# Performance work log

Hardware: AMD Instinct MI355X
Metric: run time of the kernel (lower is better)

## Reference

```python
import jax, jax.numpy as jnp
import numpy as np

N = 50000          # nodes
E = 1_600_000      # edges (avg degree 32)
H = 2              # attention heads per layer
F = 64             # per-head feature dim
NC = 16            # num_classes
NEG_SLOPE = 0.2    # PyG GATConv default leaky relu slope


def setup_inputs():
    key = jax.random.key(0)
    ks = jax.random.split(key, 20)
    s = 0.05
    z = jnp.zeros
    inp = {
        'x': jax.random.normal(ks[0], (N, 64), dtype=jnp.float32),
        'edge_index': jax.random.randint(ks[1], (2, E), 0, N, dtype=jnp.int32),
        # GAT layer 1: in=64 (heads=1 concat from input), out=H*F
        'W1': jax.random.normal(ks[2], (64, H * F)) * s,
        'a_src1': jax.random.normal(ks[3], (H, F)) * s,
        'a_dst1': jax.random.normal(ks[4], (H, F)) * s,
        'b1': z((H * F,)),
        # GAT layer 2: in=H*F=128, out=H*F
        'W2': jax.random.normal(ks[5], (H * F, H * F)) * s,
        'a_src2': jax.random.normal(ks[6], (H, F)) * s,
        'a_dst2': jax.random.normal(ks[7], (H, F)) * s,
        'b2': z((H * F,)),
        # MLP head: 128 -> 512 -> 256 -> NC
        'lw1': jax.random.normal(ks[8], (H * F, 512)) * s, 'lb1': z((512,)),
        'lw2': jax.random.normal(ks[9], (512, 256)) * s, 'lb2': z((256,)),
        'lw3': jax.random.normal(ks[10], (256, NC)) * s, 'lb3': z((NC,)),
    }
    return inp


def gat_conv(x, src, dst, W, a_src, a_dst, b):
    """PyG-style GATConv (shared weights for src/dst), head concat output."""
    h = (x @ W).reshape(-1, H, F)                       # [N, H, F]
    alpha_s = jnp.einsum('nhf,hf->nh', h, a_src)        # [N, H]
    alpha_d = jnp.einsum('nhf,hf->nh', h, a_dst)
    e = jax.nn.leaky_relu(alpha_s[src] + alpha_d[dst], NEG_SLOPE)  # [E', H]
    # segment softmax over incoming edges of each dst node
    e_max = jax.ops.segment_max(e, dst, num_segments=N)            # [N, H]
    e_exp = jnp.exp(e - e_max[dst])
    denom = jax.ops.segment_sum(e_exp, dst, num_segments=N)
    alpha = e_exp / (denom[dst] + 1e-16)                            # [E', H]
    msg = h[src] * alpha[:, :, None]                                # [E', H, F]
    out = jax.ops.segment_sum(msg, dst, num_segments=N)             # [N, H, F]
    return out.reshape(N, H * F) + b


def reference(x, edge_index, W1, a_src1, a_dst1, b1, W2, a_src2, a_dst2, b2,
              lw1, lb1, lw2, lb2, lw3, lb3):
    # add self loops (PyG GATConv default)
    loop = jnp.arange(N, dtype=edge_index.dtype)
    src = jnp.concatenate([edge_index[0], loop])
    dst = jnp.concatenate([edge_index[1], loop])

    h = jax.nn.relu(gat_conv(x, src, dst, W1, a_src1, a_dst1, b1))
    emb = jax.nn.relu(gat_conv(h, src, dst, W2, a_src2, a_dst2, b2))

    z = jax.nn.relu(emb @ lw1 + lb1)
    z = jax.nn.relu(z @ lw2 + lb2)
    logits = z @ lw3 + lb3
    return emb, logits
```

## Files before the change

kernel.cpp:

```cpp
#include <hip/hip_runtime.h>

typedef __bf16 bf16f __attribute__((ext_vector_type(8)));
typedef float  f32x4 __attribute__((ext_vector_type(4)));

__device__ __forceinline__ float bf2f(unsigned short u) {
  union { unsigned int u; float f; } v;
  v.u = ((unsigned int)u) << 16;
  return v.f;
}
__device__ __forceinline__ unsigned short f2bf(float f) {
  union { float f; unsigned int u; } v; v.f = f;
  unsigned int r = v.u + 0x7FFFu + ((v.u >> 16) & 1u);
  return (unsigned short)(r >> 16);
}
__device__ __forceinline__ float bflo(unsigned int w) {
  union { unsigned int u; float f; } v; v.u = w << 16; return v.f;
}
__device__ __forceinline__ float bfhi(unsigned int w) {
  union { unsigned int u; float f; } v; v.u = w & 0xFFFF0000u; return v.f;
}

__global__ void GNNModel_general_12077448036407_kernel(int* cnt, int ncnt) {
  int i = blockIdx.x * blockDim.x + threadIdx.x;
  if (i < ncnt) cnt[i] = 0;
}

__global__ void wpack2_kernel(const float* __restrict__ lw1, unsigned short* __restrict__ Wb1,
                              const float* __restrict__ lw2, unsigned short* __restrict__ Wb2) {
  int i = blockIdx.x * blockDim.x + threadIdx.x;
  if (i < 512 * 128) {
    int n = i >> 7, k = i & 127;
    Wb1[i] = f2bf(lw1[(size_t)k * 512 + n]);
  }
  if (i < 256 * 512) {
    int n = i >> 9, k = i & 511;
    Wb2[i] = f2bf(lw2[(size_t)k * 256 + n]);
  }
}

__launch_bounds__(256)
__global__ void gr_fused_kernel(const float* __restrict__ x, const float* __restrict__ W1,
                                unsigned short* __restrict__ hb, int M, int gblocks,
                                const int* __restrict__ dst, int* __restrict__ cnt,
                                unsigned short* __restrict__ rank, int E) {
  __shared__ float As[16][132];
  __shared__ float Bs[16][136];
  int bid = blockIdx.x;
  int t = threadIdx.x;

  if (bid >= gblocks) {
    int e = (bid - gblocks) * 256 + t;
    if (e < E) {
      int r = atomicAdd(&cnt[dst[e]], 1);
      rank[e] = (unsigned short)r;
    }
    return;
  }

  int tx = t & 15, ty = t >> 4;
  int m0 = bid * 128;

  float acc[8][8];
#pragma unroll
  for (int i = 0; i < 8; i++)
#pragma unroll
    for (int j = 0; j < 8; j++) acc[i][j] = 0.0f;

  int arow = t >> 1;
  int akc  = (t & 1) * 8;
  int bkk  = t >> 4;
  int bnn  = (t & 15) * 8;
  int gm = m0 + arow;

  for (int k0 = 0; k0 < 64; k0 += 16) {
    float av[8];
    if (gm < M) {
      const float* Af = x + (size_t)gm * 64 + k0 + akc;
      float4 r0 = *(const float4*)Af;
      float4 r1 = *(const float4*)(Af + 4);
      av[0] = r0.x; av[1] = r0.y; av[2] = r0.z; av[3] = r0.w;
      av[4] = r1.x; av[5] = r1.y; av[6] = r1.z; av[7] = r1.w;
    } else {
#pragma unroll
      for (int j = 0; j < 8; j++) av[j] = 0.0f;
    }
#pragma unroll
    for (int j = 0; j < 8; j++) As[akc + j][arow] = av[j];

    const float* bp = W1 + (size_t)(k0 + bkk) * 128 + bnn;
    float4 b0 = *(const float4*)bp;
    float4 b1 = *(const float4*)(bp + 4);
    *(float4*)&Bs[bkk][bnn]     = b0;
    *(float4*)&Bs[bkk][bnn + 4] = b1;

    __syncthreads();

#pragma unroll 4
    for (int kk = 0; kk < 16; kk++) {
      float a[8], b[8];
      *(float4*)&a[0] = *(const float4*)&As[kk][ty * 8];
      *(float4*)&a[4] = *(const float4*)&As[kk][ty * 8 + 4];
      *(float4*)&b[0] = *(const float4*)&Bs[kk][tx * 8];
      *(float4*)&b[4] = *(const float4*)&Bs[kk][tx * 8 + 4];
#pragma unroll
      for (int i = 0; i < 8; i++)
#pragma unroll
        for (int j = 0; j < 8; j++)
          acc[i][j] = fmaf(a[i], b[j], acc[i][j]);
    }
    __syncthreads();
  }

#pragma unroll
  for (int i = 0; i < 8; i++) {
    int m = m0 + ty * 8 + i;
    if (m >= M) continue;
    unsigned short* Cp = hb + (size_t)m * 128 + tx * 8;
    uint4 pk;
    pk.x = (unsigned int)f2bf(acc[i][0]) | ((unsigned int)f2bf(acc[i][1]) << 16);
    pk.y = (unsigned int)f2bf(acc[i][2]) | ((unsigned int)f2bf(acc[i][3]) << 16);
    pk.z = (unsigned int)f2bf(acc[i][4]) | ((unsigned int)f2bf(acc[i][5]) << 16);
    pk.w = (unsigned int)f2bf(acc[i][6]) | ((unsigned int)f2bf(acc[i][7]) << 16);
    *(uint4*)Cp = pk;
  }
}

__global__ void scan1_kernel(const int* __restrict__ cnt, int* __restrict__ offs,
                             int* __restrict__ bsum, int M) {
  __shared__ int sh[256];
  int t = threadIdx.x;
  int i = blockIdx.x * 256 + t;
  int v = (i < M) ? cnt[i] : 0;
  sh[t] = v;
  __syncthreads();
  for (int off = 1; off < 256; off <<= 1) {
    int u = (t >= off) ? sh[t - off] : 0;
    __syncthreads();
    sh[t] += u;
    __syncthreads();
  }
  if (i <= M) offs[i] = sh[t] - v;
  if (t == 255) bsum[blockIdx.x] = sh[255];
}

__global__ void scan2_kernel(int* __restrict__ bsum, int NB) {
  __shared__ int sh[256];
  int t = threadIdx.x;
  int v = (t < NB) ? bsum[t] : 0;
  sh[t] = v;
  __syncthreads();
  for (int off = 1; off < 256; off <<= 1) {
    int u = (t >= off) ? sh[t - off] : 0;
    __syncthreads();
    sh[t] += u;
    __syncthreads();
  }
  if (t < NB) bsum[t] = sh[t] - v;
}

__global__ void scan3_kernel(int* __restrict__ offs, const int* __restrict__ bsum, int M) {
  int i = blockIdx.x * 256 + threadIdx.x;
  if (i <= M) offs[i] += bsum[i >> 8];
}

__global__ void pa_fused_kernel(const unsigned short* __restrict__ hb,
                                const float* __restrict__ a_src,
                                const float* __restrict__ a_dst,
                                float2* __restrict__ aSp, float2* __restrict__ aDp,
                                int M, int ablocks,
                                const int* __restrict__ src, const int* __restrict__ dstp,
                                const unsigned short* __restrict__ rank,
                                const int* __restrict__ offs, int* __restrict__ csr, int E) {
  int bid = blockIdx.x;
  int t = threadIdx.x;

  if (bid >= ablocks) {
    int e = (bid - ablocks) * 256 + t;
    if (e < E) {
      int p = offs[dstp[e]] + (int)rank[e];
      __builtin_nontemporal_store(src[e], &csr[p]);
    }
    return;
  }

  int gw = (bid * 256 + t) >> 6;
  int lane = t & 63;
  if (gw >= M) return;
  float h0 = bf2f(hb[(size_t)gw * 128 + lane]);
  float h1 = bf2f(hb[(size_t)gw * 128 + 64 + lane]);
  float as0 = h0 * a_src[lane];
  float as1 = h1 * a_src[64 + lane];
  float ad0 = h0 * a_dst[lane];
  float ad1 = h1 * a_dst[64 + lane];
  for (int o = 32; o; o >>= 1) {
    as0 += __shfl_xor(as0, o);
    as1 += __shfl_xor(as1, o);
    ad0 += __shfl_xor(ad0, o);
    ad1 += __shfl_xor(ad1, o);
  }
  if (lane == 0) {
    aSp[gw] = make_float2(as0, as1);
    aDp[gw] = make_float2(ad0, ad1);
  }
}

__launch_bounds__(256)
__global__ void m128_kernel(const void* __restrict__ A,
                            const unsigned short* __restrict__ Bw,
                            const float* __restrict__ bias, void* __restrict__ C,
                            int M, int K, int Nt, int aBF, int cBF, int relu,
                            int mtiles, int lgNB) {
  __shared__ unsigned short sh[8704];
  unsigned short* As = sh;
  unsigned short* Bs = sh + 4096;
  int tid = threadIdx.x;
  int wid = tid >> 6, lane = tid & 63;
  int lm = lane & 15, quad = lane >> 4;
  int wr = wid >> 1, wc = wid & 1;

  int xcd = blockIdx.x;
  int slot = blockIdx.y;
  int qm = mtiles >> 3, rm = mtiles & 7;
  int cntm = qm + (xcd < rm);
  int mstart = xcd * qm + (xcd < rm ? xcd : rm);
  if (slot >= (cntm << lgNB)) return;
  int NBm1 = (1 << lgNB) - 1;
  int m0 = (mstart + (slot >> lgNB)) * 128;
  int n0 = (slot & NBm1) * 128;

  f32x4 acc[4][4];
#pragma unroll
  for (int mi = 0; mi < 4; mi++)
#pragma unroll
    for (int ni = 0; ni < 4; ni++)
#pragma unroll
      for (int i = 0; i < 4; i++) acc[mi][ni][i] = 0.0f;

  int c0 = (wid << 6) + lane;
  int c1 = c0 + 256;
  int srow = tid >> 1;
  int skc  = (tid & 1) << 4;

  for (int k0 = 0; k0 < K; k0 += 32) {
    {
      const unsigned short* g0 = Bw + (size_t)(n0 + (c0 >> 2)) * K + k0 + ((c0 & 3) << 3);
      __builtin_amdgcn_global_load_lds((const __attribute__((address_space(1))) void*)g0,
                                       (__attribute__((address_space(3))) void*)(Bs + (wid << 9)),
                                       16, 0, 0);
      const unsigned short* g1 = Bw + (size_t)(n0 + (c1 >> 2)) * K + k0 + ((c1 & 3) << 3);
      __builtin_amdgcn_global_load_lds((const __attribute__((address_space(1))) void*)g1,
                                       (__attribute__((address_space(3))) void*)(Bs + 2048 + (wid << 9)),
                                       16, 0, 0);
    }
    if (aBF) {
      int r0 = m0 + (c0 >> 2); if (r0 > M - 1) r0 = M - 1;
      const unsigned short* g0 = (const unsigned short*)A + (size_t)r0 * K + k0 + ((c0 & 3) << 3);
      __builtin_amdgcn_global_load_lds((const __attribute__((address_space(1))) void*)g0,
                                       (__attribute__((address_space(3))) void*)(As + (wid << 9)),
                                       16, 0, 0);
      int r1 = m0 + (c1 >> 2); if (r1 > M - 1) r1 = M - 1;
      const unsigned short* g1 = (const unsigned short*)A + (size_t)r1 * K + k0 + ((c1 & 3) << 3);
      __builtin_amdgcn_global_load_lds((const __attribute__((address_space(1))) void*)g1,
                                       (__attribute__((address_space(3))) void*)(As + 2048 + (wid << 9)),
                                       16, 0, 0);
    } else {
      int gm = m0 + srow;
      uint4 p0, p1;
      if (gm < M) {
        const float* Af = (const float*)A + (size_t)gm * K + k0 + skc;
        float4 r0 = *(const float4*)Af;
        float4 r1 = *(const float4*)(Af + 4);
        float4 r2 = *(const float4*)(Af + 8);
        float4 r3 = *(const float4*)(Af + 12);
        p0.x = (unsigned int)f2bf(r0.x) | ((unsigned int)f2bf(r0.y) << 16);
        p0.y = (unsigned int)f2bf(r0.z) | ((unsigned int)f2bf(r0.w) << 16);
        p0.z = (unsigned int)f2bf(r1.x) | ((unsigned int)f2bf(r1.y) << 16);
        p0.w = (unsigned int)f2bf(r1.z) | ((unsigned int)f2bf(r1.w) << 16);
        p1.x = (unsigned int)f2bf(r2.x) | ((unsigned int)f2bf(r2.y) << 16);
        p1.y = (unsigned int)f2bf(r2.z) | ((unsigned int)f2bf(r2.w) << 16);
        p1.z = (unsigned int)f2bf(r3.x) | ((unsigned int)f2bf(r3.y) << 16);
        p1.w = (unsigned int)f2bf(r3.z) | ((unsigned int)f2bf(r3.w) << 16);
      } else {
        p0.x = p0.y = p0.z = p0.w = 0u;
        p1.x = p1.y = p1.z = p1.w = 0u;
      }
      *(uint4*)&As[srow * 32 + skc] = p0;
      *(uint4*)&As[srow * 32 + skc + 8] = p1;
    }
    __syncthreads();

    bf16f afr[4], bfr[4];
#pragma unroll
    for (int mi = 0; mi < 4; mi++)
      afr[mi] = *(const bf16f*)&As[(wr * 64 + mi * 16 + lm) * 32 + quad * 8];
#pragma unroll
    for (int ni = 0; ni < 4; ni++)
      bfr[ni] = *(const bf16f*)&Bs[(wc * 64 + ni * 16 + lm) * 32 + quad * 8];
#pragma unroll
    for (int mi = 0; mi < 4; mi++)
#pragma unroll
      for (int ni = 0; ni < 4; ni++)
        acc[mi][ni] = __builtin_amdgcn_mfma_f32_16x16x32_bf16(afr[mi], bfr[ni], acc[mi][ni], 0, 0, 0);
    __syncthreads();
  }

  if (cBF) {
#pragma unroll
    for (int p = 0; p < 2; p++) {
      __syncthreads();
      if (wc == p) {
#pragma unroll
        for (int ni = 0; ni < 4; ni++) {
          int colb = ni * 16 + lm;
          float bv = (bias != 0) ? bias[n0 + p * 64 + colb] : 0.0f;
#pragma unroll
          for (int mi = 0; mi < 4; mi++) {
#pragma unroll
            for (int i = 0; i < 4; i++) {
              int rowb = wr * 64 + mi * 16 + quad * 4 + i;
              float v = acc[mi][ni][i] + bv;
              if (relu) v = fmaxf(v, 0.0f);
              sh[rowb * 68 + colb] = f2bf(v);
            }
          }
        }
      }
      __syncthreads();
#pragma unroll
      for (int sweep = 0; sweep < 4; sweep++) {
        int rowb = (tid >> 3) + 32 * sweep;
        int seg = tid & 7;
        int grow = m0 + rowb;
        if (grow < M) {
          uint4 val = *(const uint4*)&sh[rowb * 68 + seg * 8];
          *(uint4*)((unsigned short*)C + (size_t)grow * Nt + n0 + p * 64 + seg * 8) = val;
        }
      }
    }
  } else {
#pragma unroll
    for (int ni = 0; ni < 4; ni++) {
      int col = n0 + wc * 64 + ni * 16 + lm;
      float bv = (bias != 0) ? bias[col] : 0.0f;
#pragma unroll
      for (int mi = 0; mi < 4; mi++) {
#pragma unroll
        for (int i = 0; i < 4; i++) {
          int row = m0 + wr * 64 + mi * 16 + quad * 4 + i;
          if (row < M) {
            float v = acc[mi][ni][i] + bv;
            if (relu) v = fmaxf(v, 0.0f);
            ((float*)C)[(size_t)row * Nt + col] = v;
          }
        }
      }
    }
  }
}

__launch_bounds__(256)
__global__ void lgemm_kernel(const unsigned short* __restrict__ A,
                             const float* __restrict__ W,
                             const float* __restrict__ bias, float* __restrict__ C,
                             int M, int K) {
  __shared__ unsigned short Bt[16 * 264];
  int tid = threadIdx.x;
  int wave = tid >> 6, lane = tid & 63;
  int lm = lane & 15, quad = lane >> 4;
  int m0 = blockIdx.x * 64;

  for (int f0 = tid * 4; f0 < K * 16; f0 += 1024) {
    float4 w4 = *(const float4*)(W + f0);
    int k = f0 >> 4, n = f0 & 15;
    Bt[(n + 0) * 264 + k] = f2bf(w4.x);
    Bt[(n + 1) * 264 + k] = f2bf(w4.y);
    Bt[(n + 2) * 264 + k] = f2bf(w4.z);
    Bt[(n + 3) * 264 + k] = f2bf(w4.w);
  }
  __syncthreads();

  f32x4 acc;
#pragma unroll
  for (int i = 0; i < 4; i++) acc[i] = 0.0f;

  int m = m0 + wave * 16 + lm;
  const unsigned short* Ap = A + (size_t)m * K;

  for (int k0 = 0; k0 < K; k0 += 32) {
    bf16f af;
#pragma unroll
    for (int j = 0; j < 8; j++) af[j] = (__bf16)0.0f;
    if (m < M) af = *(const bf16f*)(Ap + k0 + quad * 8);
    bf16f bfv = *(const bf16f*)&Bt[lm * 264 + k0 + quad * 8];
    acc = __builtin_amdgcn_mfma_f32_16x16x32_bf16(af, bfv, acc, 0, 0, 0);
  }

  float bv = bias[lm];
#pragma unroll
  for (int i = 0; i < 4; i++) {
    int row = m0 + wave * 16 + quad * 4 + i;
    if (row < M) C[(size_t)row * 16 + lm] = acc[i] + bv;
  }
}

__launch_bounds__(256)
__global__ void tgemm_kernel(const void* __restrict__ A, const float* __restrict__ W,
                             const float* __restrict__ bias, void* __restrict__ C,
                             int M, int K, int Nt, int aBF, int cBF, int relu) {
  __shared__ float As[16][132];
  __shared__ float Bs[16][136];
  int t = threadIdx.x;
  int tx = t & 15, ty = t >> 4;
  int m0 = blockIdx.x * 128, n0 = blockIdx.y * 128;

  float acc[8][8];
#pragma unroll
  for (int i = 0; i < 8; i++)
#pragma unroll
    for (int j = 0; j < 8; j++) acc[i][j] = 0.0f;

  int arow = t >> 1;
  int akc  = (t & 1) * 8;
  int bkk  = t >> 4;
  int bnn  = (t & 15) * 8;
  int gm = m0 + arow;

  for (int k0 = 0; k0 < K; k0 += 16) {
    float av[8];
    if (gm < M) {
      if (aBF) {
        const unsigned short* Ab = (const unsigned short*)A + (size_t)gm * K + k0 + akc;
        uint4 raw = *(const uint4*)Ab;
        av[0] = bflo(raw.x); av[1] = bfhi(raw.x);
        av[2] = bflo(raw.y); av[3] = bfhi(raw.y);
        av[4] = bflo(raw.z); av[5] = bfhi(raw.z);
        av[6] = bflo(raw.w); av[7] = bfhi(raw.w);
      } else {
        const float* Af = (const float*)A + (size_t)gm * K + k0 + akc;
        float4 r0 = *(const float4*)Af;
        float4 r1 = *(const float4*)(Af + 4);
        av[0] = r0.x; av[1] = r0.y; av[2] = r0.z; av[3] = r0.w;
        av[4] = r1.x; av[5] = r1.y; av[6] = r1.z; av[7] = r1.w;
      }
    } else {
#pragma unroll
      for (int j = 0; j < 8; j++) av[j] = 0.0f;
    }
#pragma unroll
    for (int j = 0; j < 8; j++) As[akc + j][arow] = av[j];

    const float* bp = W + (size_t)(k0 + bkk) * Nt + n0 + bnn;
    float4 b0 = *(const float4*)bp;
    float4 b1 = *(const float4*)(bp + 4);
    *(float4*)&Bs[bkk][bnn]     = b0;
    *(float4*)&Bs[bkk][bnn + 4] = b1;

    __syncthreads();

#pragma unroll 4
    for (int kk = 0; kk < 16; kk++) {
      float a[8], b[8];
      *(float4*)&a[0] = *(const float4*)&As[kk][ty * 8];
      *(float4*)&a[4] = *(const float4*)&As[kk][ty * 8 + 4];
      *(float4*)&b[0] = *(const float4*)&Bs[kk][tx * 8];
      *(float4*)&b[4] = *(const float4*)&Bs[kk][tx * 8 + 4];
#pragma unroll
      for (int i = 0; i < 8; i++)
#pragma unroll
        for (int j = 0; j < 8; j++)
          acc[i][j] = fmaf(a[i], b[j], acc[i][j]);
    }
    __syncthreads();
  }

  float bv[8];
#pragma unroll
  for (int j = 0; j < 8; j++) bv[j] = (bias != 0) ? bias[n0 + tx * 8 + j] : 0.0f;

#pragma unroll
  for (int i = 0; i < 8; i++) {
    int m = m0 + ty * 8 + i;
    if (m >= M) continue;
    float v[8];
#pragma unroll
    for (int j = 0; j < 8; j++) {
      float s = acc[i][j] + bv[j];
      v[j] = relu ? fmaxf(s, 0.0f) : s;
    }
    if (cBF) {
      unsigned short* Cp = (unsigned short*)C + (size_t)m * Nt + n0 + tx * 8;
      uint4 pk;
      pk.x = (unsigned int)f2bf(v[0]) | ((unsigned int)f2bf(v[1]) << 16);
      pk.y = (unsigned int)f2bf(v[2]) | ((unsigned int)f2bf(v[3]) << 16);
      pk.z = (unsigned int)f2bf(v[4]) | ((unsigned int)f2bf(v[5]) << 16);
      pk.w = (unsigned int)f2bf(v[6]) | ((unsigned int)f2bf(v[7]) << 16);
      *(uint4*)Cp = pk;
    } else {
      float* Cp = (float*)C + (size_t)m * Nt + n0 + tx * 8;
      float4 o0; o0.x = v[0]; o0.y = v[1]; o0.z = v[2]; o0.w = v[3];
      float4 o1; o1.x = v[4]; o1.y = v[5]; o1.z = v[6]; o1.w = v[7];
      *(float4*)Cp = o0;
      *(float4*)(Cp + 4) = o1;
    }
  }
}

__global__ void alphas_kernel(const unsigned short* __restrict__ hb,
                              const float* __restrict__ a_src,
                              const float* __restrict__ a_dst,
                              float2* __restrict__ aSp, float2* __restrict__ aDp, int M) {
  int gw = (blockIdx.x * blockDim.x + threadIdx.x) >> 6;
  int lane = threadIdx.x & 63;
  if (gw >= M) return;
  float h0 = bf2f(hb[(size_t)gw * 128 + lane]);
  float h1 = bf2f(hb[(size_t)gw * 128 + 64 + lane]);
  float as0 = h0 * a_src[lane];
  float as1 = h1 * a_src[64 + lane];
  float ad0 = h0 * a_dst[lane];
  float ad1 = h1 * a_dst[64 + lane];
  for (int o = 32; o; o >>= 1) {
    as0 += __shfl_xor(as0, o);
    as1 += __shfl_xor(as1, o);
    ad0 += __shfl_xor(ad0, o);
    ad1 += __shfl_xor(ad1, o);
  }
  if (lane == 0) {
    aSp[gw] = make_float2(as0, as1);
    aDp[gw] = make_float2(ad0, ad1);
  }
}

__global__ void aggregate_kernel(const unsigned short* __restrict__ hb,
                                 const float2* __restrict__ aSp,
                                 const float2* __restrict__ aDp,
                                 const int* __restrict__ csr_src, const int* __restrict__ offs,
                                 const float* __restrict__ bias,
                                 float* __restrict__ out, int M) {
  int n = (blockIdx.x * blockDim.x + threadIdx.x) >> 6;
  int lane = threadIdx.x & 63;
  if (n >= M) return;
  int g = lane >> 4;
  int q = lane & 15;
  int h0sel = (q < 8);

  float2 adn = aDp[n];
  float2 asn = aSp[n];
  float e0 = asn.x + adn.x; e0 = (e0 > 0.0f) ? e0 : 0.2f * e0;
  float e1 = asn.y + adn.y; e1 = (e1 > 0.0f) ? e1 : 0.2f * e1;
  float ws0 = expf(e0), ws1 = expf(e1);
  float wself = h0sel ? ws0 : ws1;

  float acc[8];
  if (g == 0) {
    uint4 rv = *(const uint4*)(hb + (size_t)n * 128 + q * 8);
    acc[0] = wself * bflo(rv.x); acc[1] = wself * bfhi(rv.x);
    acc[2] = wself * bflo(rv.y); acc[3] = wself * bfhi(rv.y);
    acc[4] = wself * bflo(rv.z); acc[5] = wself * bfhi(rv.z);
    acc[6] = wself * bflo(rv.w); acc[7] = wself * bfhi(rv.w);
  } else {
#pragma unroll
    for (int i = 0; i < 8; i++) acc[i] = 0.0f;
  }

  float lp0 = 0.0f, lp1 = 0.0f;
  int rs = offs[n], re = offs[n + 1];
  for (int base = rs; base < re; base += 64) {
    int cnt = re - base; if (cnt > 64) cnt = 64;
    int s = 0; float w0 = 0.0f, w1 = 0.0f;
    if (lane < cnt) {
      s = csr_src[base + lane];
      float2 a = aSp[s];
      float f0 = a.x + adn.x; f0 = (f0 > 0.0f) ? f0 : 0.2f * f0;
      float f1 = a.y + adn.y; f1 = (f1 > 0.0f) ? f1 : 0.2f * f1;
      w0 = expf(f0); w1 = expf(f1);
      lp0 += w0; lp1 += w1;
    }
    int jmax = (cnt + 3) >> 2;
#pragma unroll 2
    for (int j = 0; j < jmax; j++) {
      int el = 4 * j + g;
      int sj  = __shfl(s, el);
      float w0j = __shfl(w0, el);
      float w1j = __shfl(w1, el);
      float wj = h0sel ? w0j : w1j;
      uint4 rv = *(const uint4*)(hb + (size_t)sj * 128 + q * 8);
      acc[0] = fmaf(wj, bflo(rv.x), acc[0]);
      acc[1] = fmaf(wj, bfhi(rv.x), acc[1]);
      acc[2] = fmaf(wj, bflo(rv.y), acc[2]);
      acc[3] = fmaf(wj, bfhi(rv.y), acc[3]);
      acc[4] = fmaf(wj, bflo(rv.z), acc[4]);
      acc[5] = fmaf(wj, bfhi(rv.z), acc[5]);
      acc[6] = fmaf(wj, bflo(rv.w), acc[6]);
      acc[7] = fmaf(wj, bfhi(rv.w), acc[7]);
    }
  }
#pragma unroll
  for (int i = 0; i < 8; i++) {
    acc[i] += __shfl_xor(acc[i], 16);
    acc[i] += __shfl_xor(acc[i], 32);
  }
  for (int o = 32; o; o >>= 1) {
    lp0 += __shfl_xor(lp0, o);
    lp1 += __shfl_xor(lp1, o);
  }
  if (g == 0) {
    float linv = 1.0f / ((h0sel ? lp0 + ws0 : lp1 + ws1) + 1e-16f);
    const float* bp = bias + q * 8;
    float4 o0, o1;
    o0.x = fmaxf(acc[0] * linv + bp[0], 0.0f);
    o0.y = fmaxf(acc[1] * linv + bp[1], 0.0f);
    o0.z = fmaxf(acc[2] * linv + bp[2], 0.0f);
    o0.w = fmaxf(acc[3] * linv + bp[3], 0.0f);
    o1.x = fmaxf(acc[4] * linv + bp[4], 0.0f);
    o1.y = fmaxf(acc[5] * linv + bp[5], 0.0f);
    o1.z = fmaxf(acc[6] * linv + bp[6], 0.0f);
    o1.w = fmaxf(acc[7] * linv + bp[7], 0.0f);
    float* op = out + (size_t)n * 128 + q * 8;
    *(float4*)op = o0;
    *(float4*)(op + 4) = o1;
  }
}

extern "C" void kernel_launch(void* const* d_in, const int* in_sizes, int n_in,
                              void* d_out, int out_size, void* d_ws, size_t ws_size,
                              hipStream_t stream) {
  const int N = in_sizes[0] / 64;
  const int E = in_sizes[1] / 2;
  const float* x   = (const float*)d_in[0];
  const int*   ei  = (const int*)d_in[1];
  const float* W1  = (const float*)d_in[2];
  const float* as1 = (const float*)d_in[3];
  const float* ad1 = (const float*)d_in[4];
  const float* b1  = (const float*)d_in[5];
  const float* W2  = (const float*)d_in[6];
  const float* as2 = (const float*)d_in[7];
  const float* ad2 = (const float*)d_in[8];
  const float* b2  = (const float*)d_in[9];
  const float* lw1 = (const float*)d_in[10];
  const float* lb1 = (const float*)d_in[11];
  const float* lw2 = (const float*)d_in[12];
  const float* lb2 = (const float*)d_in[13];
  const float* lw3 = (const float*)d_in[14];
  const float* lb3 = (const float*)d_in[15];

  float* emb    = (float*)d_out;
  float* logits = (float*)d_out + (size_t)N * 128;

  char* base = (char*)d_ws;
  size_t o = 0;
  unsigned short* Wb1 = (unsigned short*)(base + o); o += ((size_t)512 * 128 * 2 + 255) & ~(size_t)255;
  unsigned short* Wb2 = (unsigned short*)(base + o); o += ((size_t)256 * 512 * 2 + 255) & ~(size_t)255;
  char* tb = base + o;

  size_t t = 0;
  unsigned short* hb = (unsigned short*)(tb + t); t += ((size_t)N * 128 * 2 + 255) & ~(size_t)255;
  float* x2f = (float*)(tb + t); t += ((size_t)N * 128 * 4 + 255) & ~(size_t)255;
  float2* aSp = (float2*)(tb + t); t += ((size_t)N * 8 + 255) & ~(size_t)255;
  float2* aDp = (float2*)(tb + t); t += ((size_t)N * 8 + 255) & ~(size_t)255;
  int* cnt  = (int*)(tb + t); t += ((size_t)N * 4 + 255) & ~(size_t)255;
  int* offs = (int*)(tb + t); t += ((size_t)(N + 1) * 4 + 255) & ~(size_t)255;
  int* bsum = (int*)(tb + t); t += ((size_t)256 * 4 + 255) & ~(size_t)255;
  unsigned short* rank = (unsigned short*)(tb + t); t += ((size_t)E * 2 + 255) & ~(size_t)255;
  int* csr  = (int*)(tb + t); t += ((size_t)E * 4 + 255) & ~(size_t)255;
  unsigned short* z1b = (unsigned short*)tb;
  unsigned short* z2b = (unsigned short*)(tb + (((size_t)N * 512 * 2 + 255) & ~(size_t)255));

  const int* esrc = ei;
  const int* edst = ei + E;

  int eb = (E + 255) / 256;
  int sb = (N + 256) / 256;
  int nb4 = (N + 3) / 4;
  int mtb = (N + 127) / 128;

  GNNModel_general_12077448036407_kernel<<<(N + 255) / 256, 256, 0, stream>>>(cnt, N);
  wpack2_kernel<<<512, 256, 0, stream>>>(lw1, Wb1, lw2, Wb2);

  gr_fused_kernel<<<mtb + eb, 256, 0, stream>>>(x, W1, hb, N, mtb, edst, cnt, rank, E);

  scan1_kernel<<<sb, 256, 0, stream>>>(cnt, offs, bsum, N);
  scan2_kernel<<<1, 256, 0, stream>>>(bsum, sb);
  scan3_kernel<<<sb, 256, 0, stream>>>(offs, bsum, N);

  pa_fused_kernel<<<nb4 + eb, 256, 0, stream>>>(hb, as1, ad1, aSp, aDp, N, nb4,
                                                esrc, edst, rank, offs, csr, E);

  aggregate_kernel<<<nb4, 256, 0, stream>>>(hb, aSp, aDp, csr, offs, b1, x2f, N);

  tgemm_kernel<<<dim3(mtb, 1), 256, 0, stream>>>(x2f, W2, (const float*)0, hb,
                                                 N, 128, 128, 0, 1, 0);
  alphas_kernel<<<nb4, 256, 0, stream>>>(hb, as2, ad2, aSp, aDp, N);
  aggregate_kernel<<<nb4, 256, 0, stream>>>(hb, aSp, aDp, csr, offs, b2, emb, N);

  int qx = mtb >> 3, rx = mtb & 7;
  int spx = qx + (rx ? 1 : 0);
  m128_kernel<<<dim3(8, spx * 4), 256, 0, stream>>>(emb, Wb1, lb1, z1b,
                                                    N, 128, 512, 0, 1, 1, mtb, 2);
  m128_kernel<<<dim3(8, spx * 2), 256, 0, stream>>>(z1b, Wb2, lb2, z2b,
                                                    N, 512, 256, 1, 1, 1, mtb, 1);
  int mtb64 = (N + 63) / 64;
  lgemm_kernel<<<mtb64, 256, 0, stream>>>(z2b, lw3, lb3, logits, N, 256);
}
```

Before: 467.6 us.

## Fuse attention logits into GEMM epilogues and use split-bf16 MFMA for layer-2 GEMM

Measured after the change: 442.6 us. 5.3% less time.

```diff
diff --git a/kernel.cpp b/kernel.cpp
--- a/kernel.cpp
+++ b/kernel.cpp
@@ -25,8 +25,10 @@
   if (i < ncnt) cnt[i] = 0;
 }
 
-__global__ void wpack2_kernel(const float* __restrict__ lw1, unsigned short* __restrict__ Wb1,
-                              const float* __restrict__ lw2, unsigned short* __restrict__ Wb2) {
+__global__ void wpack3_kernel(const float* __restrict__ lw1, unsigned short* __restrict__ Wb1,
+                              const float* __restrict__ lw2, unsigned short* __restrict__ Wb2,
+                              const float* __restrict__ W2, unsigned short* __restrict__ W2h,
+                              unsigned short* __restrict__ W2l) {
   int i = blockIdx.x * blockDim.x + threadIdx.x;
   if (i < 512 * 128) {
     int n = i >> 7, k = i & 127;
@@ -36,11 +38,21 @@
     int n = i >> 9, k = i & 511;
     Wb2[i] = f2bf(lw2[(size_t)k * 256 + n]);
   }
+  if (i < 128 * 128) {
+    int n = i >> 7, k = i & 127;
+    float w = W2[(size_t)k * 128 + n];
+    unsigned short h = f2bf(w);
+    W2h[i] = h;
+    W2l[i] = f2bf(w - bf2f(h));
+  }
 }
 
 __launch_bounds__(256)
 __global__ void gr_fused_kernel(const float* __restrict__ x, const float* __restrict__ W1,
-                                unsigned short* __restrict__ hb, int M, int gblocks,
+                                unsigned short* __restrict__ hb,
+                                const float* __restrict__ a_src, const float* __restrict__ a_dst,
+                                float2* __restrict__ aSp, float2* __restrict__ aDp,
+                                int M, int gblocks,
                                 const int* __restrict__ dst, int* __restrict__ cnt,
                                 unsigned short* __restrict__ rank, int E) {
   __shared__ float As[16][132];
@@ -111,17 +123,48 @@
     __syncthreads();
   }
 
+  float aSv[8], aDv[8];
+  {
+    float4 s0 = *(const float4*)(a_src + tx * 8);
+    float4 s1 = *(const float4*)(a_src + tx * 8 + 4);
+    aSv[0]=s0.x; aSv[1]=s0.y; aSv[2]=s0.z; aSv[3]=s0.w;
+    aSv[4]=s1.x; aSv[5]=s1.y; aSv[6]=s1.z; aSv[7]=s1.w;
+    float4 d0 = *(const float4*)(a_dst + tx * 8);
+    float4 d1 = *(const float4*)(a_dst + tx * 8 + 4);
+    aDv[0]=d0.x; aDv[1]=d0.y; aDv[2]=d0.z; aDv[3]=d0.w;
+    aDv[4]=d1.x; aDv[5]=d1.y; aDv[6]=d1.z; aDv[7]=d1.w;
+  }
+
 #pragma unroll
   for (int i = 0; i < 8; i++) {
     int m = m0 + ty * 8 + i;
-    if (m >= M) continue;
-    unsigned short* Cp = hb + (size_t)m * 128 + tx * 8;
-    uint4 pk;
-    pk.x = (unsigned int)f2bf(acc[i][0]) | ((unsigned int)f2bf(acc[i][1]) << 16);
-    pk.y = (unsigned int)f2bf(acc[i][2]) | ((unsigned int)f2bf(acc[i][3]) << 16);
-    pk.z = (unsigned int)f2bf(acc[i][4]) | ((unsigned int)f2bf(acc[i][5]) << 16);
-    pk.w = (unsigned int)f2bf(acc[i][6]) | ((unsigned int)f2bf(acc[i][7]) << 16);
-    *(uint4*)Cp = pk;
+    float asP = 0.0f, adP = 0.0f;
+    if (m < M) {
+      uint4 pk;
+      pk.x = (unsigned int)f2bf(acc[i][0]) | ((unsigned int)f2bf(acc[i][1]) << 16);
+      pk.y = (unsigned int)f2bf(acc[i][2]) | ((unsigned int)f2bf(acc[i][3]) << 16);
+      pk.z = (unsigned int)f2bf(acc[i][4]) | ((unsigned int)f2bf(acc[i][5]) << 16);
+      pk.w = (unsigned int)f2bf(acc[i][6]) | ((unsigned int)f2bf(acc[i][7]) << 16);
+      *(uint4*)(hb + (size_t)m * 128 + tx * 8) = pk;
+      float av[8];
+      av[0] = bflo(pk.x); av[1] = bfhi(pk.x);
+      av[2] = bflo(pk.y); av[3] = bfhi(pk.y);
+      av[4] = bflo(pk.z); av[5] = bfhi(pk.z);
+      av[6] = bflo(pk.w); av[7] = bfhi(pk.w);
+#pragma unroll
+      for (int j = 0; j < 8; j++) {
+        asP = fmaf(av[j], aSv[j], asP);
+        adP = fmaf(av[j], aDv[j], adP);
+      }
+    }
+    asP += __shfl_xor(asP, 1); asP += __shfl_xor(asP, 2); asP += __shfl_xor(asP, 4);
+    adP += __shfl_xor(adP, 1); adP += __shfl_xor(adP, 2); adP += __shfl_xor(adP, 4);
+    float asO = __shfl_xor(asP, 8);
+    float adO = __shfl_xor(adP, 8);
+    if (m < M && tx == 0) {
+      aSp[m] = make_float2(asP, asO);
+      aDp[m] = make_float2(adP, adO);
+    }
   }
 }
 
@@ -163,44 +206,13 @@
   if (i <= M) offs[i] += bsum[i >> 8];
 }
 
-__global__ void pa_fused_kernel(const unsigned short* __restrict__ hb,
-                                const float* __restrict__ a_src,
-                                const float* __restrict__ a_dst,
-                                float2* __restrict__ aSp, float2* __restrict__ aDp,
-                                int M, int ablocks,
-                                const int* __restrict__ src, const int* __restrict__ dstp,
-                                const unsigned short* __restrict__ rank,
-                                const int* __restrict__ offs, int* __restrict__ csr, int E) {
-  int bid = blockIdx.x;
-  int t = threadIdx.x;
-
-  if (bid >= ablocks) {
-    int e = (bid - ablocks) * 256 + t;
-    if (e < E) {
-      int p = offs[dstp[e]] + (int)rank[e];
-      __builtin_nontemporal_store(src[e], &csr[p]);
-    }
-    return;
-  }
-
-  int gw = (bid * 256 + t) >> 6;
-  int lane = t & 63;
-  if (gw >= M) return;
-  float h0 = bf2f(hb[(size_t)gw * 128 + lane]);
-  float h1 = bf2f(hb[(size_t)gw * 128 + 64 + lane]);
-  float as0 = h0 * a_src[lane];
-  float as1 = h1 * a_src[64 + lane];
-  float ad0 = h0 * a_dst[lane];
-  float ad1 = h1 * a_dst[64 + lane];
-  for (int o = 32; o; o >>= 1) {
-    as0 += __shfl_xor(as0, o);
-    as1 += __shfl_xor(as1, o);
-    ad0 += __shfl_xor(ad0, o);
-    ad1 += __shfl_xor(ad1, o);
-  }
-  if (lane == 0) {
-    aSp[gw] = make_float2(as0, as1);
-    aDp[gw] = make_float2(ad0, ad1);
+__global__ void place_kernel(const int* __restrict__ src, const int* __restrict__ dst,
+                             const unsigned short* __restrict__ rank,
+                             const int* __restrict__ offs, int* __restrict__ csr_src, int E) {
+  int e = blockIdx.x * blockDim.x + threadIdx.x;
+  if (e < E) {
+    int p = offs[dst[e]] + (int)rank[e];
+    __builtin_nontemporal_store(src[e], &csr_src[p]);
   }
 }
 
@@ -359,6 +371,172 @@
 }
 
 __launch_bounds__(256)
+__global__ void tg2m_kernel(const float* __restrict__ A,
+                            const unsigned short* __restrict__ Bh,
+                            const unsigned short* __restrict__ Bl,
+                            const float* __restrict__ a_src, const float* __restrict__ a_dst,
+                            unsigned short* __restrict__ hb,
+                            float2* __restrict__ aSp, float2* __restrict__ aDp,
+                            int M) {
+  __shared__ unsigned short sh[12288];
+  unsigned short* Ah = sh;
+  unsigned short* Al = sh + 2048;
+  unsigned short* BH = sh + 4096;
+  unsigned short* BL = sh + 8192;
+  const int K = 128;
+  int tid = threadIdx.x;
+  int wid = tid >> 6, lane = tid & 63;
+  int lm = lane & 15, quad = lane >> 4;
+  int wr = wid >> 1, wc = wid & 1;
+  int m0 = blockIdx.x * 64;
+
+  f32x4 acc[2][4];
+#pragma unroll
+  for (int mi = 0; mi < 2; mi++)
+#pragma unroll
+    for (int ni = 0; ni < 4; ni++)
+#pragma unroll
+      for (int i = 0; i < 4; i++) acc[mi][ni][i] = 0.0f;
+
+  int c0 = (wid << 6) + lane, c1 = c0 + 256;
+  int srow = tid >> 2;
+  int skc = (tid & 3) << 3;
+
+  for (int k0 = 0; k0 < K; k0 += 32) {
+    {
+      const unsigned short* g0 = Bh + (size_t)(c0 >> 2) * K + k0 + ((c0 & 3) << 3);
+      __builtin_amdgcn_global_load_lds((const __attribute__((address_space(1))) void*)g0,
+                                       (__attribute__((address_space(3))) void*)(BH + (wid << 9)),
+                                       16, 0, 0);
+      const unsigned short* g1 = Bh + (size_t)(c1 >> 2) * K + k0 + ((c1 & 3) << 3);
+      __builtin_amdgcn_global_load_lds((const __attribute__((address_space(1))) void*)g1,
+                                       (__attribute__((address_space(3))) void*)(BH + 2048 + (wid << 9)),
+                                       16, 0, 0);
+      const unsigned short* g2 = Bl + (size_t)(c0 >> 2) * K + k0 + ((c0 & 3) << 3);
+      __builtin_amdgcn_global_load_lds((const __attribute__((address_space(1))) void*)g2,
+                                       (__attribute__((address_space(3))) void*)(BL + (wid << 9)),
+                                       16, 0, 0);
+      const unsigned short* g3 = Bl + (size_t)(c1 >> 2) * K + k0 + ((c1 & 3) << 3);
+      __builtin_amdgcn_global_load_lds((const __attribute__((address_space(1))) void*)g3,
+                                       (__attribute__((address_space(3))) void*)(BL + 2048 + (wid << 9)),
+                                       16, 0, 0);
+    }
+    {
+      int gm = m0 + srow;
+      uint4 ph, pl;
+      if (gm < M) {
+        const float* Af = A + (size_t)gm * K + k0 + skc;
+        float4 r0 = *(const float4*)Af;
+        float4 r1 = *(const float4*)(Af + 4);
+        float v[8] = {r0.x, r0.y, r0.z, r0.w, r1.x, r1.y, r1.z, r1.w};
+        unsigned short hh[8], ll[8];
+#pragma unroll
+        for (int j = 0; j < 8; j++) {
+          hh[j] = f2bf(v[j]);
+          ll[j] = f2bf(v[j] - bf2f(hh[j]));
+        }
+        ph.x = (unsigned int)hh[0] | ((unsigned int)hh[1] << 16);
+        ph.y = (unsigned int)hh[2] | ((unsigned int)hh[3] << 16);
+        ph.z = (unsigned int)hh[4] | ((unsigned int)hh[5] << 16);
+        ph.w = (unsigned int)hh[6] | ((unsigned int)hh[7] << 16);
+        pl.x = (unsigned int)ll[0] | ((unsigned int)ll[1] << 16);
+        pl.y = (unsigned int)ll[2] | ((unsigned int)ll[3] << 16);
+        pl.z = (unsigned int)ll[4] | ((unsigned int)ll[5] << 16);
+        pl.w = (unsigned int)ll[6] | ((unsigned int)ll[7] << 16);
+      } else {
+        ph.x = ph.y = ph.z = ph.w = 0u;
+        pl.x = pl.y = pl.z = pl.w = 0u;
+      }
+      *(uint4*)&Ah[srow * 32 + skc] = ph;
+      *(uint4*)&Al[srow * 32 + skc] = pl;
+    }
+    __syncthreads();
+
+    bf16f ahf[2], alf[2];
+#pragma unroll
+    for (int mi = 0; mi < 2; mi++) {
+      ahf[mi] = *(const bf16f*)&Ah[(wr * 32 + mi * 16 + lm) * 32 + quad * 8];
+      alf[mi] = *(const bf16f*)&Al[(wr * 32 + mi * 16 + lm) * 32 + quad * 8];
+    }
+#pragma unroll
+    for (int ni = 0; ni < 4; ni++) {
+      bf16f vbh = *(const bf16f*)&BH[(wc * 64 + ni * 16 + lm) * 32 + quad * 8];
+      bf16f vbl = *(const bf16f*)&BL[(wc * 64 + ni * 16 + lm) * 32 + quad * 8];
+#pragma unroll
+      for (int mi = 0; mi < 2; mi++) {
+        acc[mi][ni] = __builtin_amdgcn_mfma_f32_16x16x32_bf16(ahf[mi], vbh, acc[mi][ni], 0, 0, 0);
+        acc[mi][ni] = __builtin_amdgcn_mfma_f32_16x16x32_bf16(alf[mi], vbh, acc[mi][ni], 0, 0, 0);
+        acc[mi][ni] = __builtin_amdgcn_mfma_f32_16x16x32_bf16(ahf[mi], vbl, acc[mi][ni], 0, 0, 0);
+      }
+    }
+    __syncthreads();
+  }
+
+  float ps[2], pd[2];
+#pragma unroll
+  for (int p = 0; p < 2; p++) {
+    __syncthreads();
+    if (wc == p) {
+#pragma unroll
+      for (int ni = 0; ni < 4; ni++) {
+        int colb = ni * 16 + lm;
+#pragma unroll
+        for (int mi = 0; mi < 2; mi++)
+#pragma unroll
+          for (int i = 0; i < 4; i++) {
+            int rowb = wr * 32 + mi * 16 + quad * 4 + i;
+            sh[rowb * 72 + colb] = f2bf(acc[mi][ni][i]);
+          }
+      }
+    }
+    __syncthreads();
+#pragma unroll
+    for (int sweep = 0; sweep < 2; sweep++) {
+      int rowb = (tid >> 3) + 32 * sweep;
+      int seg = tid & 7;
+      int grow = m0 + rowb;
+      if (grow < M) {
+        uint4 val = *(const uint4*)&sh[rowb * 72 + seg * 8];
+        *(uint4*)(hb + (size_t)grow * 128 + p * 64 + seg * 8) = val;
+      }
+    }
+    {
+      int row = tid >> 2, sg = tid & 3;
+      const float* As_ = a_src + p * 64 + sg * 16;
+      const float* Ad_ = a_dst + p * 64 + sg * 16;
+      float s = 0.0f, d = 0.0f;
+#pragma unroll
+      for (int c8 = 0; c8 < 2; c8++) {
+        uint4 rv = *(const uint4*)&sh[row * 72 + sg * 16 + c8 * 8];
+        const float* Ap_ = As_ + c8 * 8;
+        const float* Dp_ = Ad_ + c8 * 8;
+        float hv[8];
+        hv[0] = bflo(rv.x); hv[1] = bfhi(rv.x);
+        hv[2] = bflo(rv.y); hv[3] = bfhi(rv.y);
+        hv[4] = bflo(rv.z); hv[5] = bfhi(rv.z);
+        hv[6] = bflo(rv.w); hv[7] = bfhi(rv.w);
+#pragma unroll
+        for (int j = 0; j < 8; j++) {
+          s = fmaf(hv[j], Ap_[j], s);
+          d = fmaf(hv[j], Dp_[j], d);
+        }
+      }
+      s += __shfl_xor(s, 1); s += __shfl_xor(s, 2);
+      d += __shfl_xor(d, 1); d += __shfl_xor(d, 2);
+      ps[p] = s; pd[p] = d;
+    }
+  }
+  {
+    int row = tid >> 2, sg = tid & 3;
+    int m = m0 + row;
+    if (sg == 0 && m < M) {
+      aSp[m] = make_float2(ps[0], ps[1]);
+      aDp[m] = make_float2(pd[0], pd[1]);
+    }
+  }
+}
+
+__launch_bounds__(256)
 __global__ void lgemm_kernel(const unsigned short* __restrict__ A,
                              const float* __restrict__ W,
                              const float* __restrict__ bias, float* __restrict__ C,
@@ -400,133 +578,6 @@
   for (int i = 0; i < 4; i++) {
     int row = m0 + wave * 16 + quad * 4 + i;
     if (row < M) C[(size_t)row * 16 + lm] = acc[i] + bv;
-  }
-}
-
-__launch_bounds__(256)
-__global__ void tgemm_kernel(const void* __restrict__ A, const float* __restrict__ W,
-                             const float* __restrict__ bias, void* __restrict__ C,
-                             int M, int K, int Nt, int aBF, int cBF, int relu) {
-  __shared__ float As[16][132];
-  __shared__ float Bs[16][136];
-  int t = threadIdx.x;
-  int tx = t & 15, ty = t >> 4;
-  int m0 = blockIdx.x * 128, n0 = blockIdx.y * 128;
-
-  float acc[8][8];
-#pragma unroll
-  for (int i = 0; i < 8; i++)
-#pragma unroll
-    for (int j = 0; j < 8; j++) acc[i][j] = 0.0f;
-
-  int arow = t >> 1;
-  int akc  = (t & 1) * 8;
-  int bkk  = t >> 4;
-  int bnn  = (t & 15) * 8;
-  int gm = m0 + arow;
-
-  for (int k0 = 0; k0 < K; k0 += 16) {
-    float av[8];
-    if (gm < M) {
-      if (aBF) {
-        const unsigned short* Ab = (const unsigned short*)A + (size_t)gm * K + k0 + akc;
-        uint4 raw = *(const uint4*)Ab;
-        av[0] = bflo(raw.x); av[1] = bfhi(raw.x);
-        av[2] = bflo(raw.y); av[3] = bfhi(raw.y);
-        av[4] = bflo(raw.z); av[5] = bfhi(raw.z);
-        av[6] = bflo(raw.w); av[7] = bfhi(raw.w);
-      } else {
-        const float* Af = (const float*)A + (size_t)gm * K + k0 + akc;
-        float4 r0 = *(const float4*)Af;
-        float4 r1 = *(const float4*)(Af + 4);
-        av[0] = r0.x; av[1] = r0.y; av[2] = r0.z; av[3] = r0.w;
-        av[4] = r1.x; av[5] = r1.y; av[6] = r1.z; av[7] = r1.w;
-      }
-    } else {
-#pragma unroll
-      for (int j = 0; j < 8; j++) av[j] = 0.0f;
-    }
-#pragma unroll
-    for (int j = 0; j < 8; j++) As[akc + j][arow] = av[j];
-
-    const float* bp = W + (size_t)(k0 + bkk) * Nt + n0 + bnn;
-    float4 b0 = *(const float4*)bp;
-    float4 b1 = *(const float4*)(bp + 4);
-    *(float4*)&Bs[bkk][bnn]     = b0;
-    *(float4*)&Bs[bkk][bnn + 4] = b1;
-
-    __syncthreads();
-
-#pragma unroll 4
-    for (int kk = 0; kk < 16; kk++) {
-      float a[8], b[8];
-      *(float4*)&a[0] = *(const float4*)&As[kk][ty * 8];
-      *(float4*)&a[4] = *(const float4*)&As[kk][ty * 8 + 4];
-      *(float4*)&b[0] = *(const float4*)&Bs[kk][tx * 8];
-      *(float4*)&b[4] = *(const float4*)&Bs[kk][tx * 8 + 4];
-#pragma unroll
-      for (int i = 0; i < 8; i++)
-#pragma unroll
-        for (int j = 0; j < 8; j++)
-          acc[i][j] = fmaf(a[i], b[j], acc[i][j]);
-    }
-    __syncthreads();
-  }
-
-  float bv[8];
-#pragma unroll
-  for (int j = 0; j < 8; j++) bv[j] = (bias != 0) ? bias[n0 + tx * 8 + j] : 0.0f;
-
-#pragma unroll
-  for (int i = 0; i < 8; i++) {
-    int m = m0 + ty * 8 + i;
-    if (m >= M) continue;
-    float v[8];
-#pragma unroll
-    for (int j = 0; j < 8; j++) {
-      float s = acc[i][j] + bv[j];
-      v[j] = relu ? fmaxf(s, 0.0f) : s;
-    }
-    if (cBF) {
-      unsigned short* Cp = (unsigned short*)C + (size_t)m * Nt + n0 + tx * 8;
-      uint4 pk;
-      pk.x = (unsigned int)f2bf(v[0]) | ((unsigned int)f2bf(v[1]) << 16);
-      pk.y = (unsigned int)f2bf(v[2]) | ((unsigned int)f2bf(v[3]) << 16);
-      pk.z = (unsigned int)f2bf(v[4]) | ((unsigned int)f2bf(v[5]) << 16);
-      pk.w = (unsigned int)f2bf(v[6]) | ((unsigned int)f2bf(v[7]) << 16);
-      *(uint4*)Cp = pk;
-    } else {
-      float* Cp = (float*)C + (size_t)m * Nt + n0 + tx * 8;
-      float4 o0; o0.x = v[0]; o0.y = v[1]; o0.z = v[2]; o0.w = v[3];
-      float4 o1; o1.x = v[4]; o1.y = v[5]; o1.z = v[6]; o1.w = v[7];
-      *(float4*)Cp = o0;
-      *(float4*)(Cp + 4) = o1;
-    }
-  }
-}
-
-__global__ void alphas_kernel(const unsigned short* __restrict__ hb,
-                              const float* __restrict__ a_src,
-                              const float* __restrict__ a_dst,
-                              float2* __restrict__ aSp, float2* __restrict__ aDp, int M) {
-  int gw = (blockIdx.x * blockDim.x + threadIdx.x) >> 6;
-  int lane = threadIdx.x & 63;
-  if (gw >= M) return;
-  float h0 = bf2f(hb[(size_t)gw * 128 + lane]);
-  float h1 = bf2f(hb[(size_t)gw * 128 + 64 + lane]);
-  float as0 = h0 * a_src[lane];
-  float as1 = h1 * a_src[64 + lane];
-  float ad0 = h0 * a_dst[lane];
-  float ad1 = h1 * a_dst[64 + lane];
-  for (int o = 32; o; o >>= 1) {
-    as0 += __shfl_xor(as0, o);
-    as1 += __shfl_xor(as1, o);
-    ad0 += __shfl_xor(ad0, o);
-    ad1 += __shfl_xor(ad1, o);
-  }
-  if (lane == 0) {
-    aSp[gw] = make_float2(as0, as1);
-    aDp[gw] = make_float2(ad0, ad1);
   }
 }
 
@@ -576,7 +627,7 @@
       lp0 += w0; lp1 += w1;
     }
     int jmax = (cnt + 3) >> 2;
-#pragma unroll 2
+#pragma unroll 4
     for (int j = 0; j < jmax; j++) {
       int el = 4 * j + g;
       int sj  = __shfl(s, el);
@@ -650,6 +701,8 @@
   size_t o = 0;
   unsigned short* Wb1 = (unsigned short*)(base + o); o += ((size_t)512 * 128 * 2 + 255) & ~(size_t)255;
   unsigned short* Wb2 = (unsigned short*)(base + o); o += ((size_t)256 * 512 * 2 + 255) & ~(size_t)255;
+  unsigned short* W2h = (unsigned short*)(base + o); o += ((size_t)128 * 128 * 2 + 255) & ~(size_t)255;
+  unsigned short* W2l = (unsigned short*)(base + o); o += ((size_t)128 * 128 * 2 + 255) & ~(size_t)255;
   char* tb = base + o;
 
   size_t t = 0;
@@ -672,24 +725,23 @@
   int sb = (N + 256) / 256;
   int nb4 = (N + 3) / 4;
   int mtb = (N + 127) / 128;
+  int mtb64 = (N + 63) / 64;
 
   GNNModel_general_12077448036407_kernel<<<(N + 255) / 256, 256, 0, stream>>>(cnt, N);
-  wpack2_kernel<<<512, 256, 0, stream>>>(lw1, Wb1, lw2, Wb2);
-
-  gr_fused_kernel<<<mtb + eb, 256, 0, stream>>>(x, W1, hb, N, mtb, edst, cnt, rank, E);
+  wpack3_kernel<<<512, 256, 0, stream>>>(lw1, Wb1, lw2, Wb2, W2, W2h, W2l);
+
+  gr_fused_kernel<<<mtb + eb, 256, 0, stream>>>(x, W1, hb, as1, ad1, aSp, aDp,
+                                                N, mtb, edst, cnt, rank, E);
 
   scan1_kernel<<<sb, 256, 0, stream>>>(cnt, offs, bsum, N);
   scan2_kernel<<<1, 256, 0, stream>>>(bsum, sb);
   scan3_kernel<<<sb, 256, 0, stream>>>(offs, bsum, N);
-
-  pa_fused_kernel<<<nb4 + eb, 256, 0, stream>>>(hb, as1, ad1, aSp, aDp, N, nb4,
-                                                esrc, edst, rank, offs, csr, E);
+  place_kernel<<<eb, 256, 0, stream>>>(esrc, edst, rank, offs, csr, E);
 
   aggregate_kernel<<<nb4, 256, 0, stream>>>(hb, aSp, aDp, csr, offs, b1, x2f, N);
 
-  tgemm_kernel<<<dim3(mtb, 1), 256, 0, stream>>>(x2f, W2, (const float*)0, hb,
-                                                 N, 128, 128, 0, 1, 0);
-  alphas_kernel<<<nb4, 256, 0, stream>>>(hb, as2, ad2, aSp, aDp, N);
+  tg2m_kernel<<<mtb64, 256, 0, stream>>>(x2f, W2h, W2l, as2, ad2, hb, aSp, aDp, N);
+
   aggregate_kernel<<<nb4, 256, 0, stream>>>(hb, aSp, aDp, csr, offs, b2, emb, N);
 
   int qx = mtb >> 3, rx = mtb & 7;
@@ -698,6 +750,5 @@
                                                     N, 128, 512, 0, 1, 1, mtb, 2);
   m128_kernel<<<dim3(8, spx * 2), 256, 0, stream>>>(z1b, Wb2, lb2, z2b,
                                                     N, 512, 256, 1, 1, 1, mtb, 1);
-  int mtb64 = (N + 63) / 64;
   lgemm_kernel<<<mtb64, 256, 0, stream>>>(z2b, lw3, lb3, logits, N, 256);
 }
```
